# Optimization experiments

Hardware: AMD Instinct MI355X
Metric: run time of the kernel (lower is better)

## Reference

```python
import jax, jax.numpy as jnp
import numpy as np

# Config mirrors Model(d_model=512, output_dim=2); RetNet(num_layers=2, n_heads=1)
D_MODEL = 512
N_LAYERS = 2
OUT_DIM = 2
B, S = 16, 1024
GAMMA = 1.0 - 2.0 ** -5  # RetNet decay for head 0 (n_heads=1)
EPS = 1e-6


def setup_inputs() -> dict:
    key = jax.random.key(0)
    ks = jax.random.split(key, 10)
    d, L = D_MODEL, N_LAYERS

    def rn(k, shape, scale):
        return jax.random.normal(k, shape, dtype=jnp.float32) * scale

    return {
        "x": rn(ks[0], (B, S, d), 1.0),
        # per-layer retention projections, stacked on a leading layer axis
        "Wq": rn(ks[1], (L, d, d), d ** -0.5),
        "Wk": rn(ks[2], (L, d, d), d ** -0.5),
        "Wv": rn(ks[3], (L, d, d), d ** -0.5),
        "Wg": rn(ks[4], (L, d, d), d ** -0.5),
        "Wo": rn(ks[5], (L, d, d), d ** -0.5),
        # pre-norm LayerNorm affine params
        "ln1_g": jnp.ones((L, d), jnp.float32),
        "ln1_b": jnp.zeros((L, d), jnp.float32),
        "ln2_g": jnp.ones((L, d), jnp.float32),
        "ln2_b": jnp.zeros((L, d), jnp.float32),
        # FFN (hidden = 2*d_model, gelu) per RetNet paper
        "W1": rn(ks[6], (L, d, 2 * d), d ** -0.5),
        "b1": jnp.zeros((L, 2 * d), jnp.float32),
        "W2": rn(ks[7], (L, 2 * d, d), (2 * d) ** -0.5),
        "b2": jnp.zeros((L, d), jnp.float32),
        # readout Linear(d_model, output_dim)
        "Wro": rn(ks[8], (d, OUT_DIM), d ** -0.5),
        "bro": jnp.zeros((OUT_DIM,), jnp.float32),
    }


def _layer_norm(x, g, b):
    mu = jnp.mean(x, axis=-1, keepdims=True)
    var = jnp.var(x, axis=-1, keepdims=True)
    return (x - mu) * jax.lax.rsqrt(var + EPS) * g + b


def _retention(x, Wq, Wk, Wv, Wg, Wo):
    # single head: d_head = d_model
    d = x.shape[-1]
    q = x @ Wq                      # [B,S,d]
    k = (x @ Wk) * (d ** -0.5)      # scaled keys
    v = x @ Wv
    n = jnp.arange(x.shape[1])
    diff = n[:, None] - n[None, :]
    # D[n,m] = gamma^(n-m) for n >= m else 0 (causal decay mask)
    D = jnp.where(diff >= 0, jnp.exp(diff.astype(jnp.float32) * np.log(GAMMA)), 0.0)
    scores = jnp.einsum("bnd,bmd->bnm", q, k) * D       # [B,S,S]
    ret = jnp.einsum("bnm,bmd->bnd", scores, v)          # [B,S,d]
    # GroupNorm over the (single) head dim, no affine
    mu = jnp.mean(ret, axis=-1, keepdims=True)
    var = jnp.var(ret, axis=-1, keepdims=True)
    ret = (ret - mu) * jax.lax.rsqrt(var + EPS)
    # swish gate + output projection
    return (jax.nn.silu(x @ Wg) * ret) @ Wo


def reference(x, Wq, Wk, Wv, Wg, Wo, ln1_g, ln1_b, ln2_g, ln2_b, W1, b1, W2, b2, Wro, bro):
    h = x
    for l in range(N_LAYERS):  # small fixed layer count
        h = h + _retention(_layer_norm(h, ln1_g[l], ln1_b[l]), Wq[l], Wk[l], Wv[l], Wg[l], Wo[l])
        y = _layer_norm(h, ln2_g[l], ln2_b[l])
        h = h + jax.nn.gelu(y @ W1[l] + b1[l]) @ W2[l] + b2[l]
    pooled = h.sum(axis=1)          # [B,d] sum pooling over sequence
    return pooled @ Wro + bro       # [B,OUT_DIM]
```

## Files before the change

kernel.cpp:

```cpp
#include <hip/hip_runtime.h>
#include <hip/hip_bf16.h>


#define D_MODEL 512
#define SEQ 1024
#define BATCH 16
#define NROWS (BATCH * SEQ)
#define HID 1024
#define LOG2_GAMMA (-0.04580368961f)
#define KSCALE (0.044194173824f)

typedef __attribute__((ext_vector_type(8))) short bf16x8;
typedef __attribute__((ext_vector_type(4))) float f32x4;

__device__ inline unsigned short f2bf(float x) {
    union { float f; unsigned u; } uu; uu.f = x;
    unsigned r = uu.u + 0x7fff + ((uu.u >> 16) & 1);
    return (unsigned short)(r >> 16);
}
__device__ inline float bf2f(unsigned short x) {
    union { unsigned u; float f; } uu; uu.u = ((unsigned)x) << 16; return uu.f;
}

__device__ inline void gload_lds16(const void* g, void* l) {
    __builtin_amdgcn_global_load_lds(
        (const __attribute__((address_space(1))) void*)g,
        (__attribute__((address_space(3))) void*)l, 16, 0, 0);
}

__device__ inline float sigm(float z) {
    return 1.f / (1.f + exp2f(z * -1.442695040888963f));
}
__device__ inline float gelu_fast(float x) {
    float y = 1.5957691216057308f * (x + 0.044715f * x * x * x);
    return x * sigm(y);
}

template <int EPI>
__global__ __launch_bounds__(512, 2) void gemm256p(
    const short* __restrict__ A, const short* __restrict__ B,
    const float* __restrict__ bias, unsigned short* __restrict__ C,
    int K, int lda, int ldb, int ldc, int nbx) {
    __shared__ __align__(16) short smem[4 * 16384];
    const int tid = threadIdx.x;
    const int lane = tid & 63;
    const int wid = tid >> 6;
    const int wm = wid >> 2, wn = wid & 3;
    const int cpx = gridDim.x >> 3;
    const int wg = ((int)blockIdx.x & 7) * cpx + ((int)blockIdx.x >> 3);
    const int m0 = (wg / nbx) * 256;
    const int n0 = (wg % nbx) * 256;

    const int srow = tid >> 2;
    const int scol = (((tid & 3) ^ ((tid >> 3) & 3)) * 8);
    auto stage = [&](int slot, int t) {
        int k0 = t * 32;
#pragma unroll
        for (int r = 0; r < 2; ++r) {
            gload_lds16(A + (long long)(m0 + r * 128 + srow) * lda + k0 + scol,
                        &smem[slot * 16384 + r * 4096 + wid * 512]);
            gload_lds16(B + (long long)(n0 + r * 128 + srow) * ldb + k0 + scol,
                        &smem[slot * 16384 + 8192 + r * 4096 + wid * 512]);
        }
    };

    const int NT = K >> 5;
    f32x4 acc[8][4] = {};
    const int sw8 = (((lane >> 4) ^ ((lane >> 1) & 3)) * 8);
    const int aoff = (wm * 128 + (lane & 15)) * 32 + sw8;
    const int boff = 8192 + (wn * 64 + (lane & 15)) * 32 + sw8;

    bf16x8 aR0[8], bR0[4], aR1[8], bR1[4];
    stage(0, 0); stage(1, 1); stage(2, 2);
    asm volatile("s_waitcnt vmcnt(8)" ::: "memory");
    __builtin_amdgcn_s_barrier();
#pragma unroll
    for (int m = 0; m < 8; ++m) aR0[m] = *(const bf16x8*)&smem[aoff + m * 512];
#pragma unroll
    for (int n = 0; n < 4; ++n) bR0[n] = *(const bf16x8*)&smem[boff + n * 512];

#define STEP256(T, AC, BC, AN, BN2)                                                   \
    {                                                                                 \
        int t = (T);                                                                  \
        if (t + 3 < NT) stage((t + 3) & 3, t + 3);                                    \
        if (t + 3 < NT)      asm volatile("s_waitcnt vmcnt(8)" ::: "memory");         \
        else if (t + 2 < NT) asm volatile("s_waitcnt vmcnt(4)" ::: "memory");         \
        else if (t + 1 < NT) asm volatile("s_waitcnt vmcnt(0)" ::: "memory");         \
        __builtin_amdgcn_s_barrier();                                                 \
        const int sb = ((t + 1) & 3) * 16384;                                         \
        const bool pre = (t + 1 < NT);                                                \
        _Pragma("unroll")                                                             \
        for (int q = 0; q < 4; ++q) {                                                 \
            if (pre) {                                                                \
                AN[2 * q] = *(const bf16x8*)&smem[sb + aoff + (2 * q) * 512];          \
                AN[2 * q + 1] = *(const bf16x8*)&smem[sb + aoff + (2 * q + 1) * 512];  \
                BN2[q] = *(const bf16x8*)&smem[sb + boff + q * 512];                   \
            }                                                                         \
            __builtin_amdgcn_s_setprio(1);                                            \
            _Pragma("unroll")                                                         \
            for (int n = 0; n < 4; ++n) {                                             \
                acc[2 * q][n] = __builtin_amdgcn_mfma_f32_16x16x32_bf16(AC[2 * q], BC[n], acc[2 * q][n], 0, 0, 0); \
                acc[2 * q + 1][n] = __builtin_amdgcn_mfma_f32_16x16x32_bf16(AC[2 * q + 1], BC[n], acc[2 * q + 1][n], 0, 0, 0); \
            }                                                                         \
            __builtin_amdgcn_s_setprio(0);                                            \
            __builtin_amdgcn_sched_barrier(0);                                        \
        }                                                                             \
        asm volatile("s_waitcnt lgkmcnt(0)" ::: "memory");                            \
        __builtin_amdgcn_sched_barrier(0);                                            \
    }

    for (int tt = 0; tt < NT; tt += 2) {
        STEP256(tt, aR0, bR0, aR1, bR1)
        STEP256(tt + 1, aR1, bR1, aR0, bR0)
    }
#undef STEP256

    const int ocol = lane & 15;
    const int orow4 = (lane >> 4) * 4;
    float bv[4];
    if (EPI == 2) {
#pragma unroll
        for (int n = 0; n < 4; ++n) bv[n] = bias[n0 + wn * 64 + n * 16 + ocol];
    }
#pragma unroll 1
    for (int half = 0; half < 2; ++half) {
        __syncthreads();
        if (wm == half) {
#pragma unroll
            for (int m = 0; m < 8; ++m)
#pragma unroll
                for (int n = 0; n < 4; ++n)
#pragma unroll
                    for (int rj = 0; rj < 4; ++rj) {
                        int lr = m * 16 + orow4 + rj;
                        int lc = wn * 64 + n * 16 + ocol;
                        float v = acc[m][n][rj];
                        if (EPI == 2) v = gelu_fast(v + bv[n]);
                        smem[lr * 256 + lc] = (short)f2bf(v);
                    }
        }
        __syncthreads();
#pragma unroll
        for (int p = 0; p < 8; ++p) {
            int s = p * 512 + tid;
            int row = s >> 5;
            int cc = (s & 31) * 8;
            *(int4*)&C[(long long)(m0 + half * 128 + row) * ldc + n0 + cc] =
                *(const int4*)&smem[row * 256 + cc];
        }
    }
}

template <int EPI>
__global__ __launch_bounds__(256, 2) void pgemm128(
    const short* __restrict__ A, const short* __restrict__ B,
    const float* __restrict__ bias, unsigned short* __restrict__ C,
    int K, int lda, int ldb, int ldc,
    long long sA, long long sB, long long sC, int tri) {
    __shared__ __align__(16) short smem[4 * 8192];
    const int tid = threadIdx.x;
    const int lane = tid & 63;
    const int wid = tid >> 6;
    const int wr = wid >> 1, wc = wid & 1;
    const int m0 = blockIdx.y * 128, n0 = blockIdx.x * 128;
    A += (long long)blockIdx.z * sA;
    B += (long long)blockIdx.z * sB;

    int Keff = K;
    int kstart = 0;
    if (tri) { int km = m0 + 128; if (km < Keff) Keff = km; }
    if (tri == 2) { int ks = m0 - 128; if (ks > 0) kstart = ks; }
    const int NT = (Keff - kstart) >> 5;

    auto stage = [&](int slot, int t) {
        int k0 = kstart + t * 32;
#pragma unroll
        for (int it = 0; it < 2; ++it) {
            int c = it * 256 + tid;
            int rr = c >> 2;
            int cc = ((c & 3) ^ ((c >> 3) & 3)) * 8;
            gload_lds16(A + (long long)(m0 + rr) * lda + k0 + cc,
                        &smem[slot * 8192 + (it * 256 + wid * 64) * 8]);
            gload_lds16(B + (long long)(n0 + rr) * ldb + k0 + cc,
                        &smem[slot * 8192 + 4096 + (it * 256 + wid * 64) * 8]);
        }
    };

    f32x4 acc[4][4] = {};
    const int sw8 = (((lane >> 4) ^ ((lane >> 1) & 3)) * 8);
    const int aoff = (wr * 64 + (lane & 15)) * 32 + sw8;
    const int boff = 4096 + (wc * 64 + (lane & 15)) * 32 + sw8;

    bf16x8 aR0[4], bR0[4], aR1[4], bR1[4];
    stage(0, 0); stage(1, 1); stage(2, 2);
    asm volatile("s_waitcnt vmcnt(8)" ::: "memory");
    __builtin_amdgcn_s_barrier();
#pragma unroll
    for (int m = 0; m < 4; ++m) aR0[m] = *(const bf16x8*)&smem[aoff + m * 512];
#pragma unroll
    for (int n = 0; n < 4; ++n) bR0[n] = *(const bf16x8*)&smem[boff + n * 512];

#define STEPP(T, AC, BC, AN, BN2)                                                     \
    {                                                                                 \
        int t = (T);                                                                  \
        if (t + 3 < NT) stage((t + 3) & 3, t + 3);                                    \
        if (t + 3 < NT)      asm volatile("s_waitcnt vmcnt(8)" ::: "memory");         \
        else if (t + 2 < NT) asm volatile("s_waitcnt vmcnt(4)" ::: "memory");         \
        else if (t + 1 < NT) asm volatile("s_waitcnt vmcnt(0)" ::: "memory");         \
        __builtin_amdgcn_s_barrier();                                                 \
        const int sb = ((t + 1) & 3) * 8192;                                          \
        const bool pre = (t + 1 < NT);                                                \
        _Pragma("unroll")                                                             \
        for (int q = 0; q < 4; ++q) {                                                 \
            if (pre) {                                                                \
                AN[q] = *(const bf16x8*)&smem[sb + aoff + q * 512];                    \
                BN2[q] = *(const bf16x8*)&smem[sb + boff + q * 512];                   \
            }                                                                         \
            __builtin_amdgcn_s_setprio(1);                                            \
            _Pragma("unroll")                                                         \
            for (int n = 0; n < 4; ++n)                                               \
                acc[q][n] = __builtin_amdgcn_mfma_f32_16x16x32_bf16(AC[q], BC[n], acc[q][n], 0, 0, 0); \
            __builtin_amdgcn_s_setprio(0);                                            \
            __builtin_amdgcn_sched_barrier(0);                                        \
        }                                                                             \
        asm volatile("s_waitcnt lgkmcnt(0)" ::: "memory");                            \
        __builtin_amdgcn_sched_barrier(0);                                            \
    }

    for (int tt = 0; tt < NT; tt += 2) {
        STEPP(tt, aR0, bR0, aR1, bR1)
        STEPP(tt + 1, aR1, bR1, aR0, bR0)
    }
#undef STEPP

    __syncthreads();
    const int orow = (lane >> 4) * 4;
    const int ocol = lane & 15;
    float bv[4];
    if (EPI >= 1) {
#pragma unroll
        for (int j = 0; j < 4; ++j) bv[j] = bias[n0 + wc * 64 + j * 16 + ocol];
    }
#pragma unroll
    for (int i = 0; i < 4; ++i)
#pragma unroll
        for (int j = 0; j < 4; ++j)
#pragma unroll
            for (int rj = 0; rj < 4; ++rj) {
                int lrow = wr * 64 + i * 16 + orow + rj;
                int lcol = wc * 64 + j * 16 + ocol;
                float val = acc[i][j][rj];
                if (EPI == 1) val += bv[j];
                if (EPI == 2) val = gelu_fast(val + bv[j]);
                smem[lrow * 128 + lcol] = (short)f2bf(val);
            }
    __syncthreads();
    const long long zoff = (long long)blockIdx.z * sC;
#pragma unroll
    for (int p = 0; p < 8; ++p) {
        int s = p * 256 + tid;
        int row = s >> 4;
        int cc = (s & 15) * 8;
        *(int4*)&C[zoff + (long long)(m0 + row) * ldc + n0 + cc] = *(const int4*)&smem[row * 128 + cc];
    }
}

__global__ __launch_bounds__(256, 2) void pdecay(
    const short* __restrict__ Q, const short* __restrict__ Kp,
    unsigned short* __restrict__ S, int lda, long long sA) {
    if (blockIdx.x > blockIdx.y) return;
    if (blockIdx.y > blockIdx.x + 1) return;
    const int q0 = blockIdx.y * 128;
    const int c0 = blockIdx.x * 128;
    unsigned short* Sb = S + (long long)blockIdx.z * SEQ * SEQ;
    __shared__ __align__(16) short smem[4 * 8192];
    const int tid = threadIdx.x;
    const int lane = tid & 63;
    const int wid = tid >> 6;
    const int wr = wid >> 1, wc = wid & 1;
    const short* Ab = Q + (long long)blockIdx.z * sA;
    const short* Bb = Kp + (long long)blockIdx.z * sA;

    auto stage = [&](int slot, int t) {
        int k0 = t * 32;
#pragma unroll
        for (int it = 0; it < 2; ++it) {
            int c = it * 256 + tid;
            int rr = c >> 2;
            int cc = ((c & 3) ^ ((c >> 3) & 3)) * 8;
            gload_lds16(Ab + (long long)(q0 + rr) * lda + k0 + cc,
                        &smem[slot * 8192 + (it * 256 + wid * 64) * 8]);
            gload_lds16(Bb + (long long)(c0 + rr) * lda + k0 + cc,
                        &smem[slot * 8192 + 4096 + (it * 256 + wid * 64) * 8]);
        }
    };

    const int NT = D_MODEL / 32;
    f32x4 acc[4][4] = {};
    const int sw8 = (((lane >> 4) ^ ((lane >> 1) & 3)) * 8);
    const int aoff = (wr * 64 + (lane & 15)) * 32 + sw8;
    const int boff = 4096 + (wc * 64 + (lane & 15)) * 32 + sw8;

    bf16x8 aR0[4], bR0[4], aR1[4], bR1[4];
    stage(0, 0); stage(1, 1); stage(2, 2);
    asm volatile("s_waitcnt vmcnt(8)" ::: "memory");
    __builtin_amdgcn_s_barrier();
#pragma unroll
    for (int m = 0; m < 4; ++m) aR0[m] = *(const bf16x8*)&smem[aoff + m * 512];
#pragma unroll
    for (int n = 0; n < 4; ++n) bR0[n] = *(const bf16x8*)&smem[boff + n * 512];

#define STEPD(T, AC, BC, AN, BN2)                                                     \
    {                                                                                 \
        int t = (T);                                                                  \
        if (t + 3 < NT) stage((t + 3) & 3, t + 3);                                    \
        if (t + 3 < NT)      asm volatile("s_waitcnt vmcnt(8)" ::: "memory");         \
        else if (t + 2 < NT) asm volatile("s_waitcnt vmcnt(4)" ::: "memory");         \
        else if (t + 1 < NT) asm volatile("s_waitcnt vmcnt(0)" ::: "memory");         \
        __builtin_amdgcn_s_barrier();                                                 \
        const int sb = ((t + 1) & 3) * 8192;                                          \
        const bool pre = (t + 1 < NT);                                                \
        _Pragma("unroll")                                                             \
        for (int q = 0; q < 4; ++q) {                                                 \
            if (pre) {                                                                \
                AN[q] = *(const bf16x8*)&smem[sb + aoff + q * 512];                    \
                BN2[q] = *(const bf16x8*)&smem[sb + boff + q * 512];                   \
            }                                                                         \
            __builtin_amdgcn_s_setprio(1);                                            \
            _Pragma("unroll")                                                         \
            for (int n = 0; n < 4; ++n)                                               \
                acc[q][n] = __builtin_amdgcn_mfma_f32_16x16x32_bf16(AC[q], BC[n], acc[q][n], 0, 0, 0); \
            __builtin_amdgcn_s_setprio(0);                                            \
            __builtin_amdgcn_sched_barrier(0);                                        \
        }                                                                             \
        asm volatile("s_waitcnt lgkmcnt(0)" ::: "memory");                            \
        __builtin_amdgcn_sched_barrier(0);                                            \
    }

    for (int tt = 0; tt < NT; tt += 2) {
        STEPD(tt, aR0, bR0, aR1, bR1)
        STEPD(tt + 1, aR1, bR1, aR0, bR0)
    }
#undef STEPD

    __syncthreads();
    const int orow = (lane >> 4) * 4;
    const int ocol = lane & 15;
#pragma unroll
    for (int i = 0; i < 4; ++i)
#pragma unroll
        for (int j = 0; j < 4; ++j)
#pragma unroll
            for (int rj = 0; rj < 4; ++rj) {
                int lrow = wr * 64 + i * 16 + orow + rj;
                int lcol = wc * 64 + j * 16 + ocol;
                int n = q0 + lrow, m = c0 + lcol;
                float w = (n >= m) ? exp2f((float)(n - m) * LOG2_GAMMA) * KSCALE : 0.f;
                smem[lrow * 128 + lcol] = (short)f2bf(acc[i][j][rj] * w);
            }
    __syncthreads();
#pragma unroll
    for (int p = 0; p < 8; ++p) {
        int s = p * 256 + tid;
        int row = s >> 4;
        int cc = (s & 15) * 8;
        *(int4*)&Sb[(long long)(q0 + row) * SEQ + c0 + cc] = *(const int4*)&smem[row * 128 + cc];
    }
}

__global__ __launch_bounds__(256) void wconv_all(
    const float* __restrict__ Wq, const float* __restrict__ Wk,
    const float* __restrict__ Wv, const float* __restrict__ Wg,
    const float* __restrict__ Wo, const float* __restrict__ W1,
    const float* __restrict__ W2,
    unsigned short* __restrict__ WqkvgT, unsigned short* __restrict__ WoT,
    unsigned short* __restrict__ W1T, unsigned short* __restrict__ W2T) {
    const long long dd = 512LL * 512;
    int z = blockIdx.z;
    int l = z / 7, w = z % 7;
    const float* src; unsigned short* dst; int K, N;
    switch (w) {
        case 0: src = Wq + l * dd; dst = WqkvgT + (long long)l * 4 * dd; K = 512; N = 512; break;
        case 1: src = Wk + l * dd; dst = WqkvgT + (long long)l * 4 * dd + dd; K = 512; N = 512; break;
        case 2: src = Wv + l * dd; dst = WqkvgT + (long long)l * 4 * dd + 2 * dd; K = 512; N = 512; break;
        case 3: src = Wg + l * dd; dst = WqkvgT + (long long)l * 4 * dd + 3 * dd; K = 512; N = 512; break;
        case 4: src = Wo + l * dd; dst = WoT + l * dd; K = 512; N = 512; break;
        case 5: src = W1 + (long long)l * 512 * 1024; dst = W1T + (long long)l * 512 * 1024; K = 512; N = 1024; break;
        default: src = W2 + (long long)l * 1024 * 512; dst = W2T + (long long)l * 1024 * 512; K = 1024; N = 512; break;
    }
    if ((int)blockIdx.x >= N / 64 || (int)blockIdx.y >= K / 64) return;
    __shared__ unsigned short t[64][65];
    int n0 = blockIdx.x * 64, k0 = blockIdx.y * 64;
    int tx = threadIdx.x & 63, ty = threadIdx.x >> 6;
#pragma unroll
    for (int i = 0; i < 16; ++i)
        t[ty + i * 4][tx] = f2bf(src[(long long)(k0 + ty + i * 4) * N + n0 + tx]);
    __syncthreads();
#pragma unroll
    for (int i = 0; i < 16; ++i)
        dst[(long long)(n0 + ty + i * 4) * K + k0 + tx] = t[tx][ty + i * 4];
}

__global__ __launch_bounds__(256) void vtrans(const unsigned short* __restrict__ in,
                                              unsigned short* __restrict__ out, int istride) {
    __shared__ unsigned short t[64][65];
    const unsigned short* pin = in + (long long)blockIdx.z * SEQ * istride;
    unsigned short* pout = out + (long long)blockIdx.z * D_MODEL * SEQ;
    int c0 = blockIdx.x * 64, r0 = blockIdx.y * 64;
    int tx = threadIdx.x & 63, ty = threadIdx.x >> 6;
#pragma unroll
    for (int i = 0; i < 16; ++i)
        t[ty + i * 4][tx] = pin[(long long)(r0 + ty + i * 4) * istride + c0 + tx];
    __syncthreads();
#pragma unroll
    for (int i = 0; i < 16; ++i)
        pout[(long long)(c0 + ty + i * 4) * SEQ + r0 + tx] = t[tx][ty + i * 4];
}

template <int MODE>
__global__ __launch_bounds__(256) void ln_fuse(
    const void* __restrict__ hin_v,
    const unsigned short* __restrict__ delta,
    const float* __restrict__ g, const float* __restrict__ b,
    unsigned short* __restrict__ hout,
    unsigned short* __restrict__ y) {
    int row = blockIdx.x * 4 + (threadIdx.x >> 6);
    int t = threadIdx.x & 63;
    float f[8];
    if (MODE == 2) {
        const float4* r4 = (const float4*)((const float*)hin_v + (long long)row * D_MODEL);
        float4 v0 = r4[2 * t], v1 = r4[2 * t + 1];
        f[0] = v0.x; f[1] = v0.y; f[2] = v0.z; f[3] = v0.w;
        f[4] = v1.x; f[5] = v1.y; f[6] = v1.z; f[7] = v1.w;
    } else {
        const unsigned short* hin = (const unsigned short*)hin_v;
        int4 hv = ((const int4*)(hin + (long long)row * D_MODEL))[t];
        const unsigned short* hu = (const unsigned short*)&hv;
#pragma unroll
        for (int k = 0; k < 8; ++k) f[k] = bf2f(hu[k]);
    }
    if (MODE == 1) {
        int4 dv = ((const int4*)(delta + (long long)row * D_MODEL))[t];
        const unsigned short* du = (const unsigned short*)&dv;
#pragma unroll
        for (int k = 0; k < 8; ++k) f[k] += bf2f(du[k]);
    }
    float s = 0.f, s2 = 0.f;
#pragma unroll
    for (int k = 0; k < 8; ++k) { s += f[k]; s2 += f[k] * f[k]; }
#pragma unroll
    for (int off = 32; off > 0; off >>= 1) {
        s += __shfl_down(s, off);
        s2 += __shfl_down(s2, off);
    }
    s = __shfl(s, 0); s2 = __shfl(s2, 0);
    float mu = s * (1.f / D_MODEL);
    float var = s2 * (1.f / D_MODEL) - mu * mu;
    float rs = rsqrtf(var + 1e-6f);
    if (MODE >= 1) {
        ushort4 ho[2];
        unsigned short* hp = (unsigned short*)ho;
#pragma unroll
        for (int k = 0; k < 8; ++k) hp[k] = f2bf(f[k]);
        ((int4*)(hout + (long long)row * D_MODEL))[t] = *(int4*)ho;
    }
    const float4* g4 = (const float4*)g;
    const float4* b4 = (const float4*)b;
    float4 ga = g4[2 * t], gb2 = g4[2 * t + 1];
    float4 ba = b4[2 * t], bb2 = b4[2 * t + 1];
    float gg[8] = {ga.x, ga.y, ga.z, ga.w, gb2.x, gb2.y, gb2.z, gb2.w};
    float bb[8] = {ba.x, ba.y, ba.z, ba.w, bb2.x, bb2.y, bb2.z, bb2.w};
    ushort4 yo[2];
    unsigned short* yp = (unsigned short*)yo;
#pragma unroll
    for (int k = 0; k < 8; ++k) yp[k] = f2bf((f[k] - mu) * rs * gg[k] + bb[k]);
    ((int4*)(y + (long long)row * D_MODEL))[t] = *(int4*)yo;
}

__global__ __launch_bounds__(256) void gate_bf16(const unsigned short* __restrict__ ret,
                                                 const unsigned short* __restrict__ g,
                                                 int gstride,
                                                 unsigned short* __restrict__ out) {
    int row = blockIdx.x * 4 + (threadIdx.x >> 6);
    int t = threadIdx.x & 63;
    int4 rv4 = ((const int4*)(ret + (long long)row * D_MODEL))[t];
    const unsigned short* ru = (const unsigned short*)&rv4;
    float f[8];
#pragma unroll
    for (int k = 0; k < 8; ++k) f[k] = bf2f(ru[k]);
    float s = 0.f, s2 = 0.f;
#pragma unroll
    for (int k = 0; k < 8; ++k) { s += f[k]; s2 += f[k] * f[k]; }
#pragma unroll
    for (int off = 32; off > 0; off >>= 1) {
        s += __shfl_down(s, off);
        s2 += __shfl_down(s2, off);
    }
    s = __shfl(s, 0); s2 = __shfl(s2, 0);
    float mu = s * (1.f / D_MODEL);
    float var = s2 * (1.f / D_MODEL) - mu * mu;
    float rs = rsqrtf(var + 1e-6f);
    int4 gv4 = ((const int4*)(g + (long long)row * gstride))[t];
    const unsigned short* gu = (const unsigned short*)&gv4;
    ushort4 o[2];
    unsigned short* op = (unsigned short*)o;
#pragma unroll
    for (int k = 0; k < 8; ++k) {
        float x = bf2f(gu[k]);
        op[k] = f2bf(x * sigm(x) * (f[k] - mu) * rs);
    }
    ((int4*)(out + (long long)row * D_MODEL))[t] = *(int4*)o;
}

__global__ __launch_bounds__(256) void pool_s1(const unsigned short* __restrict__ h,
                                               const unsigned short* __restrict__ d,
                                               float* __restrict__ partial) {
    int b = blockIdx.x >> 4, g = blockIdx.x & 15;
    long long base = ((long long)b * SEQ + g * 64) * D_MODEL;
    int cw = (threadIdx.x & 63) * 8;
    int rg = threadIdx.x >> 6;
    float a[8] = {};
    for (int r = rg; r < 64; r += 4) {
        long long o = base + (long long)r * D_MODEL + cw;
        int4 hv = *(const int4*)&h[o];
        int4 dv = *(const int4*)&d[o];
        const unsigned short* hp = (const unsigned short*)&hv;
        const unsigned short* dp = (const unsigned short*)&dv;
#pragma unroll
        for (int j = 0; j < 8; ++j) a[j] += bf2f(hp[j]) + bf2f(dp[j]);
    }
    __shared__ float red[4][512];
#pragma unroll
    for (int j = 0; j < 8; ++j) red[rg][cw + j] = a[j];
    __syncthreads();
#pragma unroll
    for (int cc = 0; cc < 2; ++cc) {
        int c = threadIdx.x * 2 + cc;
        partial[(long long)blockIdx.x * D_MODEL + c] =
            red[0][c] + red[1][c] + red[2][c] + red[3][c];
    }
}

__global__ __launch_bounds__(256) void pool_s2(const float* __restrict__ partial,
                                               float* __restrict__ pooled) {
    int idx = blockIdx.x * 256 + threadIdx.x;
    int b = idx >> 9, c = idx & 511;
    float s = 0.f;
#pragma unroll
    for (int g = 0; g < 16; ++g) s += partial[(long long)(b * 16 + g) * D_MODEL + c];
    pooled[idx] = s;
}

__global__ __launch_bounds__(64) void readout_kernel(const float* __restrict__ pooled,
                                                     const float* __restrict__ Wro,
                                                     const float* __restrict__ bro,
                                                     float* __restrict__ out) {
    int bo = blockIdx.x;
    int b = bo >> 1, o = bo & 1;
    int t = threadIdx.x;
    float s = 0.f;
    for (int i = t; i < D_MODEL; i += 64) s += pooled[b * D_MODEL + i] * Wro[i * 2 + o];
#pragma unroll
    for (int off = 32; off > 0; off >>= 1) s += __shfl_down(s, off);
    if (t == 0) out[b * 2 + o] = s + bro[o];
}

extern "C" void kernel_launch(void* const* d_in, const int* in_sizes, int n_in,
                              void* d_out, int out_size, void* d_ws, size_t ws_size,
                              hipStream_t stream) {
    const float* x = (const float*)d_in[0];
    const float* Wq = (const float*)d_in[1];
    const float* Wk = (const float*)d_in[2];
    const float* Wv = (const float*)d_in[3];
    const float* Wg = (const float*)d_in[4];
    const float* Wo = (const float*)d_in[5];
    const float* ln1_g = (const float*)d_in[6];
    const float* ln1_b = (const float*)d_in[7];
    const float* ln2_g = (const float*)d_in[8];
    const float* ln2_b = (const float*)d_in[9];
    const float* W1 = (const float*)d_in[10];
    const float* b1 = (const float*)d_in[11];
    const float* W2 = (const float*)d_in[12];
    const float* b2 = (const float*)d_in[13];
    const float* Wro = (const float*)d_in[14];
    const float* bro = (const float*)d_in[15];
    float* out = (float*)d_out;

    const long long NE = (long long)NROWS * D_MODEL;
    const long long dd = (long long)D_MODEL * D_MODEL;

    unsigned short* h = (unsigned short*)d_ws;
    unsigned short* y = h + NE;
    unsigned short* qkvg = y + NE;
    unsigned short* vT = qkvg + 4 * NE;
    unsigned short* gated = vT;
    unsigned short* ret = vT + NE;
    unsigned short* sg = ret + NE;
    float* pooled = (float*)(sg + 2 * NE);
    float* partial = pooled + 8192;
    unsigned short* wts = (unsigned short*)(partial + 256 * 512);
    unsigned short* WqkvgT = wts;
    unsigned short* WoT = WqkvgT + 2 * 4 * dd;
    unsigned short* W1T = WoT + 2 * dd;
    unsigned short* W2T = W1T + 2 * (long long)D_MODEL * HID;

    dim3 blk(256);
    wconv_all<<<dim3(16, 16, 14), blk, 0, stream>>>(Wq, Wk, Wv, Wg, Wo, W1, W2,
                                                    WqkvgT, WoT, W1T, W2T);

    for (int l = 0; l < 2; l++) {
        if (l == 0)
            ln_fuse<2><<<NROWS / 4, blk, 0, stream>>>(x, nullptr, ln1_g, ln1_b, h, y);
        else
            ln_fuse<1><<<NROWS / 4, blk, 0, stream>>>(h, ret, ln1_g + l * D_MODEL,
                                                      ln1_b + l * D_MODEL, h, y);
        gemm256p<0><<<512, 512, 0, stream>>>(
            (const short*)y, (const short*)(WqkvgT + (long long)l * 4 * dd), nullptr, qkvg,
            512, 512, 512, 2048, 8);
        vtrans<<<dim3(8, 16, BATCH), blk, 0, stream>>>(qkvg + 1024, vT, 2048);
        pdecay<<<dim3(8, 8, BATCH), blk, 0, stream>>>(
            (const short*)qkvg, (const short*)(qkvg + 512), sg, 2048, (long long)SEQ * 2048);
        pgemm128<0><<<dim3(4, 8, BATCH), blk, 0, stream>>>(
            (const short*)sg, (const short*)vT, nullptr, ret,
            SEQ, SEQ, SEQ, 512,
            (long long)SEQ * SEQ, (long long)D_MODEL * SEQ, (long long)SEQ * D_MODEL, 2);
        gate_bf16<<<NROWS / 4, blk, 0, stream>>>(ret, qkvg + 1536, 2048, gated);
        pgemm128<0><<<dim3(4, 128), blk, 0, stream>>>(
            (const short*)gated, (const short*)(WoT + l * dd), nullptr, sg,
            512, 512, 512, 512, 0, 0, 0, 0);
        ln_fuse<1><<<NROWS / 4, blk, 0, stream>>>(h, sg, ln2_g + l * D_MODEL,
                                                  ln2_b + l * D_MODEL, h, y);
        gemm256p<2><<<256, 512, 0, stream>>>(
            (const short*)y, (const short*)(W1T + (long long)l * D_MODEL * HID),
            b1 + l * HID, sg, 512, 512, 512, HID, 4);
        pgemm128<1><<<dim3(4, 128), blk, 0, stream>>>(
            (const short*)sg, (const short*)(W2T + (long long)l * HID * D_MODEL),
            b2 + l * D_MODEL, ret, HID, HID, HID, 512, 0, 0, 0, 0);
    }

    pool_s1<<<256, blk, 0, stream>>>(h, ret, partial);
    pool_s2<<<32, blk, 0, stream>>>(partial, pooled);
    readout_kernel<<<32, 64, 0, stream>>>(pooled, Wro, bro, out);
}
```

Baseline: 427.7 us.

## Simplify GEMM main loop to double-buffered LDS without register prefetch

Replaces the 4-slot LDS ring with 3-deep global prefetch and register double-buffering by a plain 2-slot LDS double buffer. Each iteration loads the A/B fragments from LDS and then issues MFMAs, with an extra barrier at the end. This halves LDS use (128KB to 64KB), which may improve occupancy under launch_bounds(512,2). The cost is shallower load latency hiding, no overlap of LDS reads with MFMAs, and an added barrier per K-step.

```diff
diff --git a/kernel.cpp b/kernel.cpp
--- a/kernel.cpp
+++ b/kernel.cpp
@@ -41,7 +41,7 @@
     const short* __restrict__ A, const short* __restrict__ B,
     const float* __restrict__ bias, unsigned short* __restrict__ C,
     int K, int lda, int ldb, int ldc, int nbx) {
-    __shared__ __align__(16) short smem[4 * 16384];
+    __shared__ __align__(16) short smem[2 * 16384];
     const int tid = threadIdx.x;
     const int lane = tid & 63;
     const int wid = tid >> 6;
@@ -70,50 +70,31 @@
     const int aoff = (wm * 128 + (lane & 15)) * 32 + sw8;
     const int boff = 8192 + (wn * 64 + (lane & 15)) * 32 + sw8;
 
-    bf16x8 aR0[8], bR0[4], aR1[8], bR1[4];
-    stage(0, 0); stage(1, 1); stage(2, 2);
-    asm volatile("s_waitcnt vmcnt(8)" ::: "memory");
-    __builtin_amdgcn_s_barrier();
-#pragma unroll
-    for (int m = 0; m < 8; ++m) aR0[m] = *(const bf16x8*)&smem[aoff + m * 512];
-#pragma unroll
-    for (int n = 0; n < 4; ++n) bR0[n] = *(const bf16x8*)&smem[boff + n * 512];
-
-#define STEP256(T, AC, BC, AN, BN2)                                                   \
-    {                                                                                 \
-        int t = (T);                                                                  \
-        if (t + 3 < NT) stage((t + 3) & 3, t + 3);                                    \
-        if (t + 3 < NT)      asm volatile("s_waitcnt vmcnt(8)" ::: "memory");         \
-        else if (t + 2 < NT) asm volatile("s_waitcnt vmcnt(4)" ::: "memory");         \
-        else if (t + 1 < NT) asm volatile("s_waitcnt vmcnt(0)" ::: "memory");         \
-        __builtin_amdgcn_s_barrier();                                                 \
-        const int sb = ((t + 1) & 3) * 16384;                                         \
-        const bool pre = (t + 1 < NT);                                                \
-        _Pragma("unroll")                                                             \
-        for (int q = 0; q < 4; ++q) {                                                 \
-            if (pre) {                                                                \
-                AN[2 * q] = *(const bf16x8*)&smem[sb + aoff + (2 * q) * 512];          \
-                AN[2 * q + 1] = *(const bf16x8*)&smem[sb + aoff + (2 * q + 1) * 512];  \
-                BN2[q] = *(const bf16x8*)&smem[sb + boff + q * 512];                   \
-            }                                                                         \
-            __builtin_amdgcn_s_setprio(1);                                            \
-            _Pragma("unroll")                                                         \
-            for (int n = 0; n < 4; ++n) {                                             \
-                acc[2 * q][n] = __builtin_amdgcn_mfma_f32_16x16x32_bf16(AC[2 * q], BC[n], acc[2 * q][n], 0, 0, 0); \
-                acc[2 * q + 1][n] = __builtin_amdgcn_mfma_f32_16x16x32_bf16(AC[2 * q + 1], BC[n], acc[2 * q + 1][n], 0, 0, 0); \
-            }                                                                         \
-            __builtin_amdgcn_s_setprio(0);                                            \
-            __builtin_amdgcn_sched_barrier(0);                                        \
-        }                                                                             \
-        asm volatile("s_waitcnt lgkmcnt(0)" ::: "memory");                            \
-        __builtin_amdgcn_sched_barrier(0);                                            \
-    }
-
-    for (int tt = 0; tt < NT; tt += 2) {
-        STEP256(tt, aR0, bR0, aR1, bR1)
-        STEP256(tt + 1, aR1, bR1, aR0, bR0)
-    }
-#undef STEP256
+    stage(0, 0);
+    for (int t = 0; t < NT; ++t) {
+        const int sl = t & 1;
+        if (t + 1 < NT) stage(sl ^ 1, t + 1);
+        if (t + 1 < NT) asm volatile("s_waitcnt vmcnt(4)" ::: "memory");
+        else            asm volatile("s_waitcnt vmcnt(0)" ::: "memory");
+        __builtin_amdgcn_s_barrier();
+        __builtin_amdgcn_sched_barrier(0);
+        const int sb = sl * 16384;
+        bf16x8 a[8], b[4];
+#pragma unroll
+        for (int m = 0; m < 8; ++m) a[m] = *(const bf16x8*)&smem[sb + aoff + m * 512];
+#pragma unroll
+        for (int n = 0; n < 4; ++n) b[n] = *(const bf16x8*)&smem[sb + boff + n * 512];
+        __builtin_amdgcn_s_setprio(1);
+#pragma unroll
+        for (int m = 0; m < 8; ++m)
+#pragma unroll
+            for (int n = 0; n < 4; ++n)
+                acc[m][n] = __builtin_amdgcn_mfma_f32_16x16x32_bf16(a[m], b[n], acc[m][n], 0, 0, 0);
+        __builtin_amdgcn_s_setprio(0);
+        asm volatile("s_waitcnt lgkmcnt(0)" ::: "memory");
+        __builtin_amdgcn_sched_barrier(0);
+        __builtin_amdgcn_s_barrier();
+    }
 
     const int ocol = lane & 15;
     const int orow4 = (lane >> 4) * 4;
```

After: 424.8 us. No clear change (-0.7%).
